# Kernel tuning notes

Measured on AMD Instinct MI355X. Metric: run time of the kernel, lower is better.

## Reference

```python
import jax, jax.numpy as jnp
import numpy as np
from jax.scipy.ndimage import map_coordinates

N = 512      # image H=W (x0.shape[2])
A = 30       # number of projection angles (sparse-view CT)
D = 729      # det_count (hardcoded in source)
L = 3        # LayerNo
B = 2        # batch
P = 2048     # FFT padding: next pow2 >= 2*D


def _ramp_filter(size):
    # standard Ram-Lak filter built in spatial domain (skimage/torch-radon style)
    n = np.concatenate((np.arange(1, size // 2 + 1, 2), np.arange(size // 2 - 1, 0, -2)))
    f = np.zeros(size)
    f[0] = 0.25
    f[1::2] = -1.0 / (np.pi * n) ** 2
    return jnp.asarray(2.0 * np.real(np.fft.fft(f))[: size // 2 + 1], dtype=jnp.float32)


def setup_inputs() -> dict:
    key = jax.random.key(0)
    ks = jax.random.split(key, 8)
    x0 = jax.random.normal(ks[0], (B, 1, N, N), jnp.float32)
    sinogram = jax.random.normal(ks[1], (B, 1, A, D), jnp.float32)
    theta = jnp.linspace(0.0, np.pi, A, endpoint=False).astype(jnp.float32)
    theta_label = theta
    # denoiser params, stacked over L unrolled layers
    w1 = jax.random.normal(ks[2], (L, 32, 1, 3, 3), jnp.float32) * 0.1
    b1 = jnp.zeros((L, 32), jnp.float32)
    w2 = jax.random.normal(ks[3], (L, 32, 32, 3, 3), jnp.float32) * 0.05
    b2 = jnp.zeros((L, 32), jnp.float32)
    w3 = jax.random.normal(ks[4], (L, 32, 32, 3, 3), jnp.float32) * 0.05
    b3 = jnp.zeros((L, 32), jnp.float32)
    w4 = jax.random.normal(ks[5], (L, 1, 32, 3, 3), jnp.float32) * 0.05
    steps = jnp.ones((L,), jnp.float32)  # step_n params (requires_grad=False)
    return {"cond": 1, "x0": x0, "sinogram": sinogram, "theta": theta,
            "theta_label": theta_label, "w1": w1, "b1": b1, "w2": w2, "b2": b2,
            "w3": w3, "b3": b3, "w4": w4, "steps": steps}


def _conv(x, w, b=None):
    y = jax.lax.conv_general_dilated(x, w, (1, 1), 'SAME',
                                     dimension_numbers=('NCHW', 'OIHW', 'NCHW'))
    return y if b is None else y + b[None, :, None, None]


def _denoiser(x, w1, b1, w2, b2, w3, b3, w4):
    h = jax.nn.relu(_conv(x, w1, b1))
    h = jax.nn.relu(_conv(h, w2, b2))
    h = jax.nn.relu(_conv(h, w3, b3))
    return _conv(h, w4)


def _geometry(theta):
    # parallel-beam ray sampling grid: rows/cols [A, D, T] with T=D samples (dt=1)
    c = (N - 1) / 2.0
    s = jnp.arange(D, dtype=jnp.float32) - (D - 1) / 2.0  # detector coords
    t = s                                                  # along-ray samples
    cs, sn = jnp.cos(theta), jnp.sin(theta)
    x = s[None, :, None] * cs[:, None, None] - t[None, None, :] * sn[:, None, None]
    y = s[None, :, None] * sn[:, None, None] + t[None, None, :] * cs[:, None, None]
    return y + c, x + c  # rows, cols


def _radon_fwd(imgs, rows, cols):
    # imgs [B,N,N] -> sinogram [B,A,D] via bilinear line-integral sampling
    sample = lambda im: map_coordinates(im, [rows, cols], order=1, mode='constant', cval=0.0)
    return jax.vmap(sample)(imgs).sum(-1)


def _filter_sino(sino, filt):
    F = jnp.fft.rfft(sino, n=P, axis=-1)
    g = jnp.fft.irfft(F * filt, n=P, axis=-1)[..., :D]
    return g * (jnp.pi / (2.0 * A))  # FBP normalization


def _backproj(sino, theta):
    # sino [B,A,D] -> image [B,N,N], linear interp along detector axis
    c = (N - 1) / 2.0
    xs = jnp.arange(N, dtype=jnp.float32) - c
    cs, sn = jnp.cos(theta), jnp.sin(theta)
    sgrid = cs[:, None, None] * xs[None, None, :] + sn[:, None, None] * xs[None, :, None]  # [A,N,N]
    idx = sgrid + (D - 1) / 2.0
    lo = jnp.floor(idx).astype(jnp.int32)
    w = idx - lo
    lo_ok = (lo >= 0) & (lo < D)
    hi_ok = (lo + 1 >= 0) & (lo + 1 < D)
    lo_c = jnp.clip(lo, 0, D - 1)
    hi_c = jnp.clip(lo + 1, 0, D - 1)
    a = jnp.arange(A)[:, None, None]
    v = sino[:, a, lo_c] * jnp.where(lo_ok, 1.0 - w, 0.0) + \
        sino[:, a, hi_c] * jnp.where(hi_ok, w, 0.0)       # [B,A,N,N]
    return v.sum(axis=1)


def reference(cond, x0, sinogram, theta, theta_label, w1, b1, w2, b2, w3, b3, w4, steps):
    rows, cols = _geometry(theta)
    filt = _ramp_filter(P)
    X = x0[:, 0]           # [B,N,N]
    sino = sinogram[:, 0]  # [B,A,D]
    for n in range(L):
        sino_pred = _radon_fwd(X, rows, cols)
        filtered = _filter_sino(sino_pred, filt)
        outputs = _backproj(sino - filtered, theta)
        z = X + steps[n] * outputs
        noise = _denoiser(X[:, None], w1[n], b1[n], w2[n], b2[n], w3[n], b3[n], w4[n])[:, 0]
        filtered_noise = _filter_sino(_radon_fwd(noise, rows, cols), filt)
        outputs_noise = _backproj(filtered_noise, theta)
        X = z + noise - steps[n] * outputs_noise
    Xo = X[:, None]
    return (Xo, Xo, Xo)
```

## Files before the change

### kernel.cpp

```cpp
#include <hip/hip_runtime.h>
#include <hip/hip_bf16.h>

typedef __hip_bfloat16 bf16;
typedef __attribute__((ext_vector_type(8))) short short8;
typedef __attribute__((ext_vector_type(4))) short s4v;
typedef __attribute__((ext_vector_type(4))) float float4v;

#define NN 512
#define NA 30
#define ND 729
#define NB 2
#define NL 3
#define BNN (NB*NN*NN)
#define BAD (NB*NA*ND)

#define PW 520
#define PH 516
#define PIMG (PH*PW)
#define POFF (2*PW + 2)

#define O_CS  0
#define O_SN  32
#define O_ICS 64
#define O_ISN 96
#define O_XP  128
#define O_YP  (O_XP + 2*PIMG)
#define O_YPT (O_YP + 2*PIMG)
#define O_SP  (O_YPT + 2*PIMG)
#define O_Q   (O_SP + BAD)
#define O_WR  (O_Q + BAD)
#define O_H   (((O_WR + 34560) + 15) & ~15)
#define H_FLOATS (NB * 32 * NN * NN / 2)

#define WR2_OFF 0
#define WR3_OFF 27648
#define WR4_OFF 55296

__device__ __forceinline__ float2 ld2u(const float* p)
{
    float2 r;
    __builtin_memcpy(&r, p, 8);
    return r;
}

__global__ void k_prep(const float* __restrict__ theta,
                       const float* __restrict__ w2, const float* __restrict__ w3,
                       const float* __restrict__ w4, const float* __restrict__ x0,
                       float* __restrict__ ws, bf16* __restrict__ wr)
{
    int idx = blockIdx.x * 256 + threadIdx.x;
    if (idx < NA) {
        float t = theta[idx];
        float cs = cosf(t), sn = sinf(t);
        ws[O_CS + idx] = cs;
        ws[O_SN + idx] = sn;
        ws[O_ICS + idx] = 1.0f / cs;
        ws[O_ISN + idx] = -1.0f / sn;
    }
    if (idx < 2 * 27648) {
        const float* w = (idx < 27648) ? w2 : w3;
        int base = (idx < 27648) ? WR2_OFF : WR3_OFF;
        int r = idx % 27648;
        int n = r / 9216; int r2 = r % 9216;
        int tap = r2 / 1024; int r3 = r2 % 1024;
        int co = r3 / 32, ci = r3 % 32;
        wr[base + r] = __float2bfloat16(w[n * 9216 + (co * 32 + ci) * 9 + tap]);
    } else if (idx < 2 * 27648 + 3 * 4608) {
        int r = idx - 2 * 27648;
        int n = r / 4608; int r2 = r % 4608;
        int tap = r2 / 512; int r3 = r2 % 512;
        int co = r3 / 32, ci = r3 % 32;
        float v = (co == 0) ? w4[n * 288 + ci * 9 + tap] : 0.f;
        wr[WR4_OFF + r] = __float2bfloat16(v);
    }
    if (idx < 2 * PIMG) {
        int b = idx / PIMG, p = idx % PIMG;
        int y = p / PW, x = p % PW;
        bool interior = (y >= 2 && y < 2 + NN && x >= 2 && x < 2 + NN);
        float v = interior ? x0[b * NN * NN + (y - 2) * NN + (x - 2)] : 0.f;
        ws[O_XP + idx] = v;
        if (!interior) {
            ws[O_YP + idx] = 0.f;
            ws[O_YPT + idx] = 0.f;
        }
    }
}

__device__ __forceinline__ void isect2(float A, float inv, float lo, float hi,
                                       float& tlo, float& thi)
{
    float a = (lo - A) * inv, b = (hi - A) * inv;
    tlo = fmaxf(tlo, fminf(a, b));
    thi = fminf(thi, fmaxf(a, b));
}

__global__ __launch_bounds__(256) void k_radon(const float* __restrict__ img,
    const float* __restrict__ imgT, const float* __restrict__ ws,
    float* __restrict__ out)
{
    int b = blockIdx.z, a = blockIdx.y;
    int wave = threadIdx.x >> 6;
    int lane = threadIdx.x & 63;
    int half = lane >> 5, tl = lane & 31;
    int s = blockIdx.x * 8 + wave * 2 + half;
    float cs = ws[O_CS + a], sn = ws[O_SN + a];
    float ics = ws[O_ICS + a], isn = ws[O_ISN + a];
    float s_c = (float)s - 364.0f;
    float A_r = 255.5f + s_c * sn;
    float A_c = 255.5f + s_c * cs;

    float tlo = -1e9f, thi = 1e9f;
    isect2(A_r, ics, -1.0f, 512.0f, tlo, thi);
    isect2(A_c, isn, -1.0f, 512.0f, tlo, thi);
    float t0f = fmaxf(tlo + 364.0f, 0.0f);
    float t1f = fminf(thi + 364.0f, 728.0f);

    bool useT = fabsf(cs) >= fabsf(sn);
    const float* im = (useT ? imgT : img) + b * PIMG;

    float acc = 0.f;
    if (s < ND && t0f <= t1f) {
        int tb = (int)ceilf(t0f);
        int te = (int)floorf(t1f);
#pragma unroll 2
        for (int t = tb + tl; t <= te; t += 32) {
            float tc = (float)t - 364.0f;
            float r = fmaf(tc, cs, A_r);
            float c = fmaf(-tc, sn, A_c);
            float rf = floorf(r), cf = floorf(c);
            float dr = r - rf, dc = c - cf;
            int irr = (int)rf, icc = (int)cf;
            int idx = useT ? (icc * PW + irr) : (irr * PW + icc);
            float da = useT ? dr : dc;
            float db = useT ? dc : dr;
            float2 p1 = ld2u(im + idx);
            float2 p2 = ld2u(im + idx + PW);
            float u = fmaf(da, p1.y - p1.x, p1.x);
            float w = fmaf(da, p2.y - p2.x, p2.x);
            acc = fmaf(db, w - u, acc + u);
        }
    }
    acc += __shfl_xor(acc, 16, 64);
    acc += __shfl_xor(acc, 8, 64);
    acc += __shfl_xor(acc, 4, 64);
    acc += __shfl_xor(acc, 2, 64);
    acc += __shfl_xor(acc, 1, 64);
    if (tl == 0 && s < ND) out[(b * NA + a) * ND + s] = acc;
}

__global__ void k_filter(const float* __restrict__ sp, const float* __restrict__ sino,
                         float* __restrict__ q)
{
    __shared__ float row[ND];
    __shared__ float taps[364];
    int ba = blockIdx.y;
    const float* src = sp + ba * ND;
    for (int i = threadIdx.x; i < ND; i += 256) row[i] = src[i];
    const float PI2 = 9.86960440108936f;
    for (int i = threadIdx.x; i < 364; i += 256) {
        float m = (float)(2 * i + 1);
        taps[i] = -2.0f / (PI2 * m * m);
    }
    __syncthreads();
    const float scale = 0.0523598775598299f;
    int d = blockIdx.x * 256 + threadIdx.x;
    if (d < ND) {
        float g0 = 0.5f * row[d], g1 = 0.f;
#pragma unroll 4
        for (int j = 0; j < 364; j += 2) {
            int m0 = 2 * j + 1, m1 = 2 * j + 3;
            float l0 = (d - m0 >= 0) ? row[d - m0] : 0.f;
            float r0 = (d + m0 < ND) ? row[d + m0] : 0.f;
            g0 = fmaf(taps[j], l0 + r0, g0);
            float l1 = (d - m1 >= 0) ? row[d - m1] : 0.f;
            float r1 = (d + m1 < ND) ? row[d + m1] : 0.f;
            g1 = fmaf(taps[j + 1], l1 + r1, g1);
        }
        q[ba * ND + d] = sino[ba * ND + d] - scale * (g0 + g1);
    }
}

__global__ __launch_bounds__(256) void k_backproj_update(const float* __restrict__ q,
    const float* __restrict__ src1, const float* __restrict__ ws,
    const float* __restrict__ steps, int n, float* __restrict__ out,
    float* __restrict__ outcopy)
{
    __shared__ float qt[NA][28];
    __shared__ int dmin_s[NA];
    int b = blockIdx.z;
    int x0 = blockIdx.x * 16, y0 = blockIdx.y * 16;
    int tid = threadIdx.x;
    int lx = tid & 15, ly = tid >> 4;
    const float* qb = q + b * NA * ND;

    for (int idx = tid; idx < NA * 26; idx += 256) {
        int a = idx / 26, j = idx % 26;
        float cs = ws[O_CS + a], sn = ws[O_SN + a];
        float f00 = fmaf(cs, (float)x0 - 255.5f, fmaf(sn, (float)y0 - 255.5f, 364.0f));
        float fmn = f00 + fminf(cs * 15.f, 0.f) + fminf(sn * 15.f, 0.f);
        int dm = (int)floorf(fmn);
        if (j == 0) dmin_s[a] = dm;
        int d = dm + j;
        qt[a][j] = (d >= 0 && d < ND) ? qb[a * ND + d] : 0.f;
    }
    __syncthreads();

    float xc = (float)(x0 + lx) - 255.5f, yc = (float)(y0 + ly) - 255.5f;
    float acc = 0.f;
#pragma unroll
    for (int a = 0; a < NA; a++) {
        float cs = ws[O_CS + a], sn = ws[O_SN + a];
        float f = fmaf(cs, xc, fmaf(sn, yc, 364.0f));
        float lf = floorf(f);
        float w = f - lf;
        int j = (int)lf - dmin_s[a];
        float v0 = qt[a][j], v1 = qt[a][j + 1];
        acc = fmaf(v0, 1.0f - w, fmaf(v1, w, acc));
    }
    int pidx = b * PIMG + (y0 + ly) * PW + (x0 + lx);
    float v = fmaf(steps[n], acc, src1[pidx]);
    out[pidx] = v;
    if (outcopy) {
        int fidx = b * NN * NN + (y0 + ly) * NN + (x0 + lx);
        outcopy[fidx] = v;
        outcopy[fidx + BNN] = v;
        outcopy[fidx + 2 * BNN] = v;
    }
}

__global__ __launch_bounds__(256) void k_conv12(const float* __restrict__ XPb,
    const float* __restrict__ W1, const float* __restrict__ B1,
    const bf16* __restrict__ Wr2, const float* __restrict__ B2,
    bf16* __restrict__ outb)
{
    __shared__ bf16 h1t[34][18][32];
    int b = blockIdx.z;
    int x0 = blockIdx.x * 16;
    int Y0 = blockIdx.y * 32;
    const float* in = XPb + b * PIMG;

    for (int p = threadIdx.x; p < 34 * 18; p += 256) {
        int yy = p / 18, xx = p % 18;
        int gy = Y0 + yy - 1, gx = x0 + xx - 1;
        if (gy < 0 || gy >= NN || gx < 0 || gx >= NN) {
#pragma unroll
            for (int g = 0; g < 4; g++)
                *(short8*)(&h1t[yy][xx][g * 8]) = short8{};
        } else {
            float v[9];
#pragma unroll
            for (int dy = 0; dy < 3; dy++)
#pragma unroll
                for (int dx = 0; dx < 3; dx++)
                    v[dy * 3 + dx] = in[(gy + dy - 1) * PW + (gx + dx - 1)];
#pragma unroll
            for (int g = 0; g < 4; g++) {
                short8 pk;
#pragma unroll
                for (int j = 0; j < 8; j++) {
                    int co = g * 8 + j;
                    float a = B1[co];
                    const float* w = W1 + co * 9;
#pragma unroll
                    for (int k = 0; k < 9; k++) a = fmaf(v[k], w[k], a);
                    a = fmaxf(a, 0.f);
                    bf16 h = __float2bfloat16(a);
                    pk[j] = *reinterpret_cast<short*>(&h);
                }
                *(short8*)(&h1t[yy][xx][g * 8]) = pk;
            }
        }
    }
    __syncthreads();

    int lane = threadIdx.x & 63;
    int wave = threadIdx.x >> 6;
    int n16 = lane & 15, quad = lane >> 4;
    int y0w = Y0 + wave * 8;

    short8 wf[18];
#pragma unroll
    for (int tap = 0; tap < 9; tap++)
#pragma unroll
        for (int t = 0; t < 2; t++)
            wf[tap * 2 + t] = *(const short8*)(Wr2 + ((tap * 2 + t) * 16 + n16) * 32 + quad * 8);

    short8 win[3][3];
    auto loadrow = [&](int yy, short8* dst) {
        int ly = yy - (Y0 - 1);
#pragma unroll
        for (int dx = 0; dx < 3; dx++)
            dst[dx] = *(const short8*)(&h1t[ly][n16 + dx][quad * 8]);
    };
    loadrow(y0w - 1, win[0]);
    loadrow(y0w,     win[1]);

    float4v bias[2];
#pragma unroll
    for (int t = 0; t < 2; t++)
        bias[t] = *(const float4v*)(B2 + t * 16 + quad * 4);

    bf16* out = outb + (size_t)b * NN * NN * 32;
#pragma unroll
    for (int i = 0; i < 8; i++) {
        int y = y0w + i;
        loadrow(y + 1, win[(i + 2) % 3]);
        float4v acc[2];
#pragma unroll
        for (int t = 0; t < 2; t++) acc[t] = bias[t];
#pragma unroll
        for (int dy = 0; dy < 3; dy++) {
            short8* row = win[(i + dy) % 3];
#pragma unroll
            for (int dx = 0; dx < 3; dx++) {
                int tap = dy * 3 + dx;
#pragma unroll
                for (int t = 0; t < 2; t++)
                    acc[t] = __builtin_amdgcn_mfma_f32_16x16x32_bf16(wf[tap * 2 + t], row[dx], acc[t], 0, 0, 0);
            }
        }
        bf16* pp = out + ((size_t)y * NN + x0 + n16) * 32 + quad * 4;
#pragma unroll
        for (int t = 0; t < 2; t++) {
            s4v pk;
#pragma unroll
            for (int r = 0; r < 4; r++) {
                float v = fmaxf(acc[t][r], 0.f);
                bf16 h = __float2bfloat16(v);
                pk[r] = *reinterpret_cast<short*>(&h);
            }
            *(s4v*)(pp + t * 16) = pk;
        }
    }
}

#define C34_W 64
#define C34_H 8
#define C34_PX 66
#define H3S 40

__global__ __launch_bounds__(320, 3) void k_conv34(const bf16* __restrict__ inb,
    const bf16* __restrict__ Wr3, const float* __restrict__ B3,
    const bf16* __restrict__ Wr4, const float* __restrict__ addsrc,
    float* __restrict__ outY, float* __restrict__ outT)
{
    __shared__ bf16 h3s[10][C34_PX][H3S];
    int lane = threadIdx.x & 63;
    int wave = threadIdx.x >> 6;
    int n16 = lane & 15, quad = lane >> 4;
    int b = blockIdx.z;
    int x0 = blockIdx.x * C34_W;
    int y0 = blockIdx.y * C34_H;
    const bf16* in = inb + (size_t)b * NN * NN * 32;

    {
        short8 wf3[18];
#pragma unroll
        for (int tap = 0; tap < 9; tap++)
#pragma unroll
            for (int t = 0; t < 2; t++)
                wf3[tap * 2 + t] = *(const short8*)(Wr3 + ((tap * 2 + t) * 16 + n16) * 32 + quad * 8);
        float4v bias3[2];
#pragma unroll
        for (int t = 0; t < 2; t++)
            bias3[t] = *(const float4v*)(B3 + t * 16 + quad * 4);

        int pxi = wave * 16 + n16;
        int gx0 = x0 + pxi - 2;
        bool cvx[3];
#pragma unroll
        for (int dx = 0; dx < 3; dx++) {
            int gx = gx0 + dx;
            cvx[dx] = (gx >= 0) && (gx < NN);
        }
        bool pxok = pxi < C34_PX;
        int gcol = x0 + pxi - 1;
        bool colv = pxok && (gcol >= 0) && (gcol < NN);

        short8 win[3][3];
        auto ldrow = [&](int gy, short8* dst) {
            if (gy >= 0 && gy < NN) {
                const bf16* rowp = in + (size_t)gy * NN * 32 + quad * 8;
#pragma unroll
                for (int dx = 0; dx < 3; dx++) {
                    short8 v = {};
                    if (cvx[dx]) v = *(const short8*)(rowp + (size_t)(gx0 + dx) * 32);
                    dst[dx] = v;
                }
            } else {
                dst[0] = short8{}; dst[1] = short8{}; dst[2] = short8{};
            }
        };
        ldrow(y0 - 2, win[0]);
        ldrow(y0 - 1, win[1]);
#pragma unroll
        for (int r = 0; r < 10; r++) {
            int hy = y0 - 1 + r;
            ldrow(hy + 1, win[(r + 2) % 3]);
            float4v a3[2] = {bias3[0], bias3[1]};
#pragma unroll
            for (int dy = 0; dy < 3; dy++) {
                short8* row = win[(r + dy) % 3];
#pragma unroll
                for (int dx = 0; dx < 3; dx++) {
                    int tap = dy * 3 + dx;
#pragma unroll
                    for (int t = 0; t < 2; t++)
                        a3[t] = __builtin_amdgcn_mfma_f32_16x16x32_bf16(wf3[tap * 2 + t], row[dx], a3[t], 0, 0, 0);
                }
            }
            bool rowv = (hy >= 0) && (hy < NN);
            bool live = rowv && colv;
            if (pxok) {
#pragma unroll
                for (int t = 0; t < 2; t++) {
                    s4v pk = {};
                    if (live) {
#pragma unroll
                        for (int r2 = 0; r2 < 4; r2++) {
                            float v = fmaxf(a3[t][r2], 0.f);
                            bf16 h = __float2bfloat16(v);
                            pk[r2] = *reinterpret_cast<short*>(&h);
                        }
                    }
                    *(s4v*)(&h3s[r][pxi][t * 16 + quad * 4]) = pk;
                }
            }
        }
    }
    __syncthreads();

    if (wave < 4) {
        short8 wf4[9];
#pragma unroll
        for (int tap = 0; tap < 9; tap++)
            wf4[tap] = *(const short8*)(Wr4 + (tap * 16 + n16) * 32 + quad * 8);

        int c = wave * 16 + n16;
        short8 hw[3][3];
        auto ldh = [&](int r, short8* dst) {
#pragma unroll
            for (int dx = 0; dx < 3; dx++)
                dst[dx] = *(const short8*)(&h3s[r][c + dx][quad * 8]);
        };
        ldh(0, hw[0]);
        ldh(1, hw[1]);
#pragma unroll
        for (int i = 0; i < 8; i++) {
            ldh(i + 2, hw[(i + 2) % 3]);
            float4v a4 = {0.f, 0.f, 0.f, 0.f};
#pragma unroll
            for (int dy = 0; dy < 3; dy++) {
                short8* row = hw[(i + dy) % 3];
#pragma unroll
                for (int dx = 0; dx < 3; dx++)
                    a4 = __builtin_amdgcn_mfma_f32_16x16x32_bf16(wf4[dy * 3 + dx], row[dx], a4, 0, 0, 0);
            }
            if (quad == 0) {
                int px = x0 + c;
                int y = y0 + i;
                int pidx = b * PIMG + y * PW + px;
                float vv = addsrc[pidx] + a4[0];
                outY[pidx] = vv;
                outT[b * PIMG + px * PW + y] = vv;
            }
        }
    }
}

extern "C" void kernel_launch(void* const* d_in, const int* in_sizes, int n_in,
                              void* d_out, int out_size, void* d_ws, size_t ws_size,
                              hipStream_t stream)
{
    const float* x0    = (const float*)d_in[1];
    const float* sg    = (const float*)d_in[2];
    const float* theta = (const float*)d_in[3];
    const float* w1    = (const float*)d_in[5];
    const float* b1    = (const float*)d_in[6];
    const float* w2    = (const float*)d_in[7];
    const float* b2    = (const float*)d_in[8];
    const float* w3    = (const float*)d_in[9];
    const float* b3    = (const float*)d_in[10];
    const float* w4    = (const float*)d_in[11];
    const float* steps = (const float*)d_in[12];

    float* ws = (float*)d_ws;
    float* XP  = ws + O_XP + POFF;
    float* YP  = ws + O_YP + POFF;
    float* YPT = ws + O_YPT + POFF;
    float* SP = ws + O_SP;
    float* Q  = ws + O_Q;
    bf16* wr  = (bf16*)(ws + O_WR);
    bf16* h2  = (bf16*)(ws + O_H + H_FLOATS);

    k_prep<<<(2 * PIMG + 255) / 256, 256, 0, stream>>>(theta, w2, w3, w4, x0, ws, wr);

    for (int n = 0; n < NL; n++) {
        k_conv12<<<dim3(32, 16, NB), 256, 0, stream>>>(
            XP, w1 + n * 288, b1 + n * 32, wr + WR2_OFF + n * 9216, b2 + n * 32, h2);
        k_conv34<<<dim3(8, 64, NB), 320, 0, stream>>>(
            h2, wr + WR3_OFF + n * 9216, b3 + n * 32, wr + WR4_OFF + n * 4608,
            XP, YP, YPT);

        k_radon<<<dim3((ND + 7) / 8, NA, NB), 256, 0, stream>>>(YP, YPT, ws, SP);
        k_filter<<<dim3(3, NB * NA), 256, 0, stream>>>(SP, sg, Q);
        k_backproj_update<<<dim3(32, 32, NB), 256, 0, stream>>>(
            Q, YP, ws, steps, n, XP, (n == NL - 1) ? (float*)d_out : nullptr);
    }
}
```

Baseline: 413.5 us.

## Fuse conv3 and conv4 in registers via cross-lane permutes instead of LDS

Rewrites the conv3+conv4 kernel so that each wave computes conv3 for a 16-pixel strip with one pixel of halo on each side and writes 14 output pixels. The conv3 activations are repacked into MFMA B-operand layout with ds_bpermute and kept in a three-row register ring, and conv4 horizontal taps are summed through lane shuffles. This removes the shared-memory staging buffer, the block barrier and the idle waves in the second stage. In exchange it recomputes halo pixels (16 lanes for 14 outputs), issues more bpermute traffic and raises register pressure.

```diff
diff --git a/kernel.cpp b/kernel.cpp
--- a/kernel.cpp
+++ b/kernel.cpp
@@ -5,6 +5,7 @@
 typedef __attribute__((ext_vector_type(8))) short short8;
 typedef __attribute__((ext_vector_type(4))) short s4v;
 typedef __attribute__((ext_vector_type(4))) float float4v;
+typedef __attribute__((ext_vector_type(4))) int int4v;
 
 #define NN 512
 #define NA 30
@@ -41,6 +42,14 @@
     float2 r;
     __builtin_memcpy(&r, p, 8);
     return r;
+}
+
+__device__ __forceinline__ unsigned pk2(float x, float y)
+{
+    bf16 a = __float2bfloat16(x);
+    bf16 b = __float2bfloat16(y);
+    return (unsigned)*reinterpret_cast<unsigned short*>(&a)
+         | ((unsigned)*reinterpret_cast<unsigned short*>(&b) << 16);
 }
 
 __global__ void k_prep(const float* __restrict__ theta,
@@ -334,135 +343,133 @@
     }
 }
 
-#define C34_W 64
-#define C34_H 8
-#define C34_PX 66
-#define H3S 40
-
-__global__ __launch_bounds__(320, 3) void k_conv34(const bf16* __restrict__ inb,
+__global__ __launch_bounds__(256) void k_conv34(const bf16* __restrict__ inb,
     const bf16* __restrict__ Wr3, const float* __restrict__ B3,
     const bf16* __restrict__ Wr4, const float* __restrict__ addsrc,
     float* __restrict__ outY, float* __restrict__ outT)
 {
-    __shared__ bf16 h3s[10][C34_PX][H3S];
     int lane = threadIdx.x & 63;
     int wave = threadIdx.x >> 6;
     int n16 = lane & 15, quad = lane >> 4;
     int b = blockIdx.z;
-    int x0 = blockIdx.x * C34_W;
-    int y0 = blockIdx.y * C34_H;
+    int y0 = blockIdx.y * 8;
+    int s = blockIdx.x * 4 + wave;
+    int pxbase = 14 * s - 1;
     const bf16* in = inb + (size_t)b * NN * NN * 32;
 
-    {
-        short8 wf3[18];
-#pragma unroll
-        for (int tap = 0; tap < 9; tap++)
-#pragma unroll
-            for (int t = 0; t < 2; t++)
-                wf3[tap * 2 + t] = *(const short8*)(Wr3 + ((tap * 2 + t) * 16 + n16) * 32 + quad * 8);
-        float4v bias3[2];
+    short8 wf3[18];
+#pragma unroll
+    for (int tap = 0; tap < 9; tap++)
 #pragma unroll
         for (int t = 0; t < 2; t++)
-            bias3[t] = *(const float4v*)(B3 + t * 16 + quad * 4);
-
-        int pxi = wave * 16 + n16;
-        int gx0 = x0 + pxi - 2;
-        bool cvx[3];
-#pragma unroll
-        for (int dx = 0; dx < 3; dx++) {
-            int gx = gx0 + dx;
-            cvx[dx] = (gx >= 0) && (gx < NN);
-        }
-        bool pxok = pxi < C34_PX;
-        int gcol = x0 + pxi - 1;
-        bool colv = pxok && (gcol >= 0) && (gcol < NN);
-
-        short8 win[3][3];
-        auto ldrow = [&](int gy, short8* dst) {
-            if (gy >= 0 && gy < NN) {
-                const bf16* rowp = in + (size_t)gy * NN * 32 + quad * 8;
-#pragma unroll
-                for (int dx = 0; dx < 3; dx++) {
-                    short8 v = {};
-                    if (cvx[dx]) v = *(const short8*)(rowp + (size_t)(gx0 + dx) * 32);
-                    dst[dx] = v;
+            wf3[tap * 2 + t] = *(const short8*)(Wr3 + ((tap * 2 + t) * 16 + n16) * 32 + quad * 8);
+    short8 wf4[9];
+#pragma unroll
+    for (int tap = 0; tap < 9; tap++)
+        wf4[tap] = *(const short8*)(Wr4 + (tap * 16 + n16) * 32 + quad * 8);
+    float4v bias3[2];
+#pragma unroll
+    for (int t = 0; t < 2; t++)
+        bias3[t] = *(const float4v*)(B3 + t * 16 + quad * 4);
+
+    int hpx = pxbase + n16;
+    bool hvx = (hpx >= 0) && (hpx < NN);
+    int gx0 = hpx - 1;
+    bool cvx[3];
+#pragma unroll
+    for (int dx = 0; dx < 3; dx++) {
+        int gx = gx0 + dx;
+        cvx[dx] = (gx >= 0) && (gx < NN);
+    }
+
+    short8 win[3][3];
+    auto ldrow = [&](int gy, short8* dst) {
+        if (gy >= 0 && gy < NN) {
+            const bf16* rowp = in + (size_t)gy * NN * 32 + quad * 8;
+#pragma unroll
+            for (int dx = 0; dx < 3; dx++) {
+                short8 v = {};
+                if (cvx[dx]) v = *(const short8*)(rowp + (size_t)(gx0 + dx) * 32);
+                dst[dx] = v;
+            }
+        } else {
+            dst[0] = short8{}; dst[1] = short8{}; dst[2] = short8{};
+        }
+    };
+    ldrow(y0 - 2, win[0]);
+    ldrow(y0 - 1, win[1]);
+
+    int idx_lo = (n16 + 32 * (quad & 1)) * 4;
+    int idx_hi = idx_lo + 64;
+    int idx_m1 = (lane - 1) * 4;
+    int idx_p1 = (lane + 1) * 4;
+    bool hi2 = quad >= 2;
+
+    short8 Bring[3];
+    bool svalid = s < 37;
+
+#pragma unroll
+    for (int k = 0; k < 10; k++) {
+        int hy = y0 - 1 + k;
+        ldrow(hy + 1, win[(k + 2) % 3]);
+        float4v a3[2] = {bias3[0], bias3[1]};
+#pragma unroll
+        for (int dy = 0; dy < 3; dy++) {
+            short8* row = win[(k + dy) % 3];
+#pragma unroll
+            for (int dx = 0; dx < 3; dx++) {
+                int tap = dy * 3 + dx;
+#pragma unroll
+                for (int t = 0; t < 2; t++)
+                    a3[t] = __builtin_amdgcn_mfma_f32_16x16x32_bf16(wf3[tap * 2 + t], row[dx], a3[t], 0, 0, 0);
+            }
+        }
+        bool live = hvx && (hy >= 0) && (hy < NN);
+        unsigned p00 = 0, p01 = 0, p10 = 0, p11 = 0;
+        if (live) {
+            p00 = pk2(fmaxf(a3[0][0], 0.f), fmaxf(a3[0][1], 0.f));
+            p01 = pk2(fmaxf(a3[0][2], 0.f), fmaxf(a3[0][3], 0.f));
+            p10 = pk2(fmaxf(a3[1][0], 0.f), fmaxf(a3[1][1], 0.f));
+            p11 = pk2(fmaxf(a3[1][2], 0.f), fmaxf(a3[1][3], 0.f));
+        }
+        int q0a = __builtin_amdgcn_ds_bpermute(idx_lo, (int)p00);
+        int q1a = __builtin_amdgcn_ds_bpermute(idx_lo, (int)p01);
+        int q2a = __builtin_amdgcn_ds_bpermute(idx_hi, (int)p00);
+        int q3a = __builtin_amdgcn_ds_bpermute(idx_hi, (int)p01);
+        int q0b = __builtin_amdgcn_ds_bpermute(idx_lo, (int)p10);
+        int q1b = __builtin_amdgcn_ds_bpermute(idx_lo, (int)p11);
+        int q2b = __builtin_amdgcn_ds_bpermute(idx_hi, (int)p10);
+        int q3b = __builtin_amdgcn_ds_bpermute(idx_hi, (int)p11);
+        int4v bw;
+        bw[0] = hi2 ? q0b : q0a;
+        bw[1] = hi2 ? q1b : q1a;
+        bw[2] = hi2 ? q2b : q2a;
+        bw[3] = hi2 ? q3b : q3a;
+        Bring[k % 3] = *reinterpret_cast<short8*>(&bw);
+
+        if (k >= 2) {
+            int y = y0 + k - 2;
+            float4v acc4[3];
+#pragma unroll
+            for (int dx = 0; dx < 3; dx++) acc4[dx] = (float4v){0.f, 0.f, 0.f, 0.f};
+#pragma unroll
+            for (int dy = 0; dy < 3; dy++) {
+                short8 row = Bring[(k - 2 + dy) % 3];
+#pragma unroll
+                for (int dx = 0; dx < 3; dx++)
+                    acc4[dx] = __builtin_amdgcn_mfma_f32_16x16x32_bf16(wf4[dy * 3 + dx], row, acc4[dx], 0, 0, 0);
+            }
+            float sl = __int_as_float(__builtin_amdgcn_ds_bpermute(idx_m1, __float_as_int(acc4[0][0])));
+            float sr = __int_as_float(__builtin_amdgcn_ds_bpermute(idx_p1, __float_as_int(acc4[2][0])));
+            float sum = sl + acc4[1][0] + sr;
+            if (quad == 0 && n16 >= 1 && n16 <= 14 && svalid) {
+                int ox = pxbase + n16;
+                if (ox < NN) {
+                    int pidx = b * PIMG + y * PW + ox;
+                    float vv = addsrc[pidx] + sum;
+                    outY[pidx] = vv;
+                    outT[b * PIMG + ox * PW + y] = vv;
                 }
-            } else {
-                dst[0] = short8{}; dst[1] = short8{}; dst[2] = short8{};
-            }
-        };
-        ldrow(y0 - 2, win[0]);
-        ldrow(y0 - 1, win[1]);
-#pragma unroll
-        for (int r = 0; r < 10; r++) {
-            int hy = y0 - 1 + r;
-            ldrow(hy + 1, win[(r + 2) % 3]);
-            float4v a3[2] = {bias3[0], bias3[1]};
-#pragma unroll
-            for (int dy = 0; dy < 3; dy++) {
-                short8* row = win[(r + dy) % 3];
-#pragma unroll
-                for (int dx = 0; dx < 3; dx++) {
-                    int tap = dy * 3 + dx;
-#pragma unroll
-                    for (int t = 0; t < 2; t++)
-                        a3[t] = __builtin_amdgcn_mfma_f32_16x16x32_bf16(wf3[tap * 2 + t], row[dx], a3[t], 0, 0, 0);
-                }
-            }
-            bool rowv = (hy >= 0) && (hy < NN);
-            bool live = rowv && colv;
-            if (pxok) {
-#pragma unroll
-                for (int t = 0; t < 2; t++) {
-                    s4v pk = {};
-                    if (live) {
-#pragma unroll
-                        for (int r2 = 0; r2 < 4; r2++) {
-                            float v = fmaxf(a3[t][r2], 0.f);
-                            bf16 h = __float2bfloat16(v);
-                            pk[r2] = *reinterpret_cast<short*>(&h);
-                        }
-                    }
-                    *(s4v*)(&h3s[r][pxi][t * 16 + quad * 4]) = pk;
-                }
-            }
-        }
-    }
-    __syncthreads();
-
-    if (wave < 4) {
-        short8 wf4[9];
-#pragma unroll
-        for (int tap = 0; tap < 9; tap++)
-            wf4[tap] = *(const short8*)(Wr4 + (tap * 16 + n16) * 32 + quad * 8);
-
-        int c = wave * 16 + n16;
-        short8 hw[3][3];
-        auto ldh = [&](int r, short8* dst) {
-#pragma unroll
-            for (int dx = 0; dx < 3; dx++)
-                dst[dx] = *(const short8*)(&h3s[r][c + dx][quad * 8]);
-        };
-        ldh(0, hw[0]);
-        ldh(1, hw[1]);
-#pragma unroll
-        for (int i = 0; i < 8; i++) {
-            ldh(i + 2, hw[(i + 2) % 3]);
-            float4v a4 = {0.f, 0.f, 0.f, 0.f};
-#pragma unroll
-            for (int dy = 0; dy < 3; dy++) {
-                short8* row = hw[(i + dy) % 3];
-#pragma unroll
-                for (int dx = 0; dx < 3; dx++)
-                    a4 = __builtin_amdgcn_mfma_f32_16x16x32_bf16(wf4[dy * 3 + dx], row[dx], a4, 0, 0, 0);
-            }
-            if (quad == 0) {
-                int px = x0 + c;
-                int y = y0 + i;
-                int pidx = b * PIMG + y * PW + px;
-                float vv = addsrc[pidx] + a4[0];
-                outY[pidx] = vv;
-                outT[b * PIMG + px * PW + y] = vv;
             }
         }
     }
@@ -498,7 +505,7 @@
     for (int n = 0; n < NL; n++) {
         k_conv12<<<dim3(32, 16, NB), 256, 0, stream>>>(
             XP, w1 + n * 288, b1 + n * 32, wr + WR2_OFF + n * 9216, b2 + n * 32, h2);
-        k_conv34<<<dim3(8, 64, NB), 320, 0, stream>>>(
+        k_conv34<<<dim3(10, 64, NB), 256, 0, stream>>>(
             h2, wr + WR3_OFF + n * 9216, b3 + n * 32, wr + WR4_OFF + n * 4608,
             XP, YP, YPT);
 
```

Measured after the change: 422.8 us. 1.02x slower.
